# Optimization experiments

Measured on AMD Instinct MI355X. Metric: run time of the kernel, lower is better.

The kernel has to match this reference:

```python
import jax, jax.numpy as jnp
import numpy as np

B, T, C, HS = 4, 2048, 1024, 64

def setup_inputs() -> dict:
    key = jax.random.key(0)
    k1, k2, k3, k4 = jax.random.split(key, 4)
    # weights stored as [n_embd, head_size] so projection is x @ W
    scale = C ** -0.5
    return {
        "x": jax.random.normal(k1, (B, T, C), dtype=jnp.float32),
        "Wq": jax.random.normal(k2, (C, HS), dtype=jnp.float32) * scale,
        "Wk": jax.random.normal(k3, (C, HS), dtype=jnp.float32) * scale,
        "Wv": jax.random.normal(k4, (C, HS), dtype=jnp.float32) * scale,
    }

def reference(x, Wq, Wk, Wv):
    # single-head causal attention: softmax(QK^T / sqrt(hs)) V, dropout p=0 (eval)
    q = x @ Wq  # [B,T,hs]
    k = x @ Wk
    v = x @ Wv
    hs = k.shape[-1]
    wei = jnp.einsum('bqh,bkh->bqk', q, k) * (hs ** -0.5)  # [B,T,T]
    causal = jnp.tril(jnp.ones((q.shape[1], q.shape[1]), dtype=bool))
    wei = jnp.where(causal[None, :, :], wei, -jnp.inf)
    wei = jax.nn.softmax(wei, axis=-1)
    out = jnp.einsum('bqk,bkh->bqh', wei, v)  # [B,T,hs]
    return out
```

## Files before the change

### kernel.cpp

```cpp
#include <hip/hip_runtime.h>
#include <stdint.h>

#define NB 4
#define NT 2048
#define NC 1024
#define NH 64
#define NM (NB*NT)

typedef unsigned short u16;
typedef unsigned int u32;
typedef __bf16 bf16_t;
typedef float f32x4 __attribute__((ext_vector_type(4)));
typedef bf16_t bf16x8 __attribute__((ext_vector_type(8)));
typedef u16 u16x8 __attribute__((ext_vector_type(8)));
typedef u16 u16x4 __attribute__((ext_vector_type(4)));

__device__ __forceinline__ u16 f2b(float f) {
  return __builtin_bit_cast(u16, (bf16_t)f);
}

__device__ __forceinline__ void gl16(const void* g, void* l) {
  __builtin_amdgcn_global_load_lds(
      (const __attribute__((address_space(1))) u32*)g,
      (__attribute__((address_space(3))) u32*)l, 16, 0, 0);
}

__global__ __launch_bounds__(256) void wt_kernel(const float* __restrict__ Wq,
                                                 const float* __restrict__ Wk,
                                                 const float* __restrict__ Wv,
                                                 u16* __restrict__ wt) {
  __shared__ float t[64][65];
  const int m = blockIdx.x >> 4;
  const int kt = blockIdx.x & 15;
  const int k0 = kt * 64;
  const float* W = (m == 0) ? Wq : (m == 1) ? Wk : Wv;
  {
    const int r = threadIdx.x >> 2, c4 = threadIdx.x & 3;
    #pragma unroll
    for (int j = 0; j < 4; ++j) {
      const float4 f = *(const float4*)(W + (size_t)(k0 + r) * NH + c4 * 16 + j * 4);
      t[r][c4 * 16 + j * 4 + 0] = f.x;
      t[r][c4 * 16 + j * 4 + 1] = f.y;
      t[r][c4 * 16 + j * 4 + 2] = f.z;
      t[r][c4 * 16 + j * 4 + 3] = f.w;
    }
  }
  __syncthreads();
  const int n = threadIdx.x >> 2, kc = threadIdx.x & 3;
  u16x8 a, b;
  #pragma unroll
  for (int j = 0; j < 8; ++j) a[j] = f2b(t[kc * 16 + j][n]);
  #pragma unroll
  for (int j = 0; j < 8; ++j) b[j] = f2b(t[kc * 16 + 8 + j][n]);
  u16* dst = wt + ((size_t)(m * 64 + n)) * NC + k0 + kc * 16;
  *(u16x8*)dst = a;
  *(u16x8*)(dst + 8) = b;
}

__global__ __launch_bounds__(512) void proj_kernel(const float* __restrict__ x,
                                                   const u16* __restrict__ wt,
                                                   u16* __restrict__ qo,
                                                   u16* __restrict__ ko,
                                                   u16* __restrict__ vto) {
  __shared__ float fA[2][32 * 64];
  __shared__ u16 sB[2][64 * 64];
  const int tid = threadIdx.x;
  const int lane = tid & 63;
  const int wv = tid >> 6;
  const int rt = wv & 1;
  const int w = wv >> 1;
  const int g = lane >> 4;
  const int li = lane & 15;
  const int row0 = blockIdx.x * 32;
  const int m = blockIdx.y;
  const int wbase16 = (tid & 0x1C0) * 16;
  const u16* wslice = wt + (size_t)m * 64 * NC;

  const f32x4 zero = {0.f, 0.f, 0.f, 0.f};
  f32x4 acc = zero;

  const int ar = tid >> 4, ac = tid & 15;
  const int bn = tid >> 3, bc = tid & 7;
  const float* asrc = x + (size_t)(row0 + ar) * NC + ((ac ^ (ar & 7)) * 4);
  const u16* bsrc = wslice + (size_t)bn * NC + ((bc ^ (bn & 7)) * 8);

  auto stage = [&](int kt, int nxt) {
    const int k0 = kt * 64;
    gl16(asrc + k0, (char*)fA[nxt] + wbase16 + (lane << 4));
    gl16(bsrc + k0, (char*)sB[nxt] + wbase16 + (lane << 4));
  };

  stage(0, 0);
  __syncthreads();

  for (int kt = 0; kt < 16; ++kt) {
    const int cur = kt & 1;
    if (kt < 15) stage(kt + 1, cur ^ 1);
    #pragma unroll
    for (int ks = 0; ks < 2; ++ks) {
      const int n = w * 16 + li;
      const bf16x8 b = *(const bf16x8*)&sB[cur][n * 64 + (((ks * 4 + g) ^ (n & 7)) * 8)];
      const int r = rt * 16 + li;
      const int c0 = ks * 8 + g * 2;
      const f32x4 a0 = *(const f32x4*)&fA[cur][r * 64 + ((c0 ^ (r & 7)) * 4)];
      const f32x4 a1 = *(const f32x4*)&fA[cur][r * 64 + (((c0 + 1) ^ (r & 7)) * 4)];
      bf16x8 a;
      a[0]=(bf16_t)a0.x; a[1]=(bf16_t)a0.y; a[2]=(bf16_t)a0.z; a[3]=(bf16_t)a0.w;
      a[4]=(bf16_t)a1.x; a[5]=(bf16_t)a1.y; a[6]=(bf16_t)a1.z; a[7]=(bf16_t)a1.w;
      acc = __builtin_amdgcn_mfma_f32_16x16x32_bf16(a, b, acc, 0, 0, 0);
    }
    __syncthreads();
  }

  const int rr0 = row0 + rt * 16 + g * 4;
  if (m == 0) {
    #pragma unroll
    for (int i = 0; i < 4; ++i)
      qo[(size_t)(rr0 + i) * NH + w * 16 + li] = f2b(acc[i]);
  } else if (m == 1) {
    #pragma unroll
    for (int i = 0; i < 4; ++i)
      ko[(size_t)(rr0 + i) * NH + w * 16 + li] = f2b(acc[i]);
  } else {
    u16x4 pv;
    #pragma unroll
    for (int i = 0; i < 4; ++i) pv[i] = f2b(acc[i]);
    const int hs = w * 16 + li;
    const int bidx = rr0 >> 11;
    const int tt = rr0 & 2047;
    const int tile = tt >> 6, off = tt & 63;
    *(u16x4*)&vto[(((size_t)(bidx * 32 + tile) * 64) + hs) * 64 + off] = pv;
  }
}

struct AttnGrp {
  union {
    struct { u16 K[2][32 * 64]; u16 V[2][64 * 32]; } st;
    struct { float mo[2][16][64]; float ml[2][16]; } mg;
  } u;
};

__global__ __launch_bounds__(512) void attn_kernel(const u16* __restrict__ qg,
                                                   const u16* __restrict__ kg,
                                                   const u16* __restrict__ vtg,
                                                   float* __restrict__ out) {
  __shared__ AttnGrp grp[8];
  __shared__ u16 sP[8][16 * 32];
  const int tid = threadIdx.x;
  const int lane = tid & 63;
  const int s = tid >> 6;
  const int g = lane >> 4;
  const int li = lane & 15;
  const int jA = blockIdx.x & 63;
  const int bb = blockIdx.x >> 6;
  const int jB = 127 - jA;
  const size_t bt0 = (size_t)bb * NT;
  const int q0A = jA * 16, q0B = jB * 16;
  const int n1 = (jA >> 1) + 1;

  bf16x8 aqA[2], aqB[2];
  #pragma unroll
  for (int ks = 0; ks < 2; ++ks) {
    aqA[ks] = *(const bf16x8*)(qg + (bt0 + q0A + li) * NH + ks * 32 + g * 8);
    aqB[ks] = *(const bf16x8*)(qg + (bt0 + q0B + li) * NH + ks * 32 + g * 8);
  }

  const f32x4 zero = {0.f, 0.f, 0.f, 0.f};
  f32x4 oA[4], oB[4];
  float lA[4], lB[4];
  #pragma unroll
  for (int i = 0; i < 4; ++i) { oA[i] = zero; oB[i] = zero; lA[i] = 0.f; lB[i] = 0.f; }

  auto stageKV = [&](int v, int b) {
    const int kvt = (v < n1) ? v : v - n1;
    const size_t kbase = bt0 + (size_t)kvt * 32;
    #pragma unroll
    for (int jj = 0; jj < 4; ++jj) {
      const int idx = jj * 64 + lane;
      const int n = idx >> 3, c = idx & 7;
      gl16(kg + (kbase + n) * NH + ((c ^ (n & 7)) * 8),
           (char*)grp[s].u.st.K[b] + jj * 1024);
    }
    const size_t vbase = ((size_t)(bb * 32 + (kvt >> 1))) * 64;
    const int hoff = (kvt & 1) * 32;
    #pragma unroll
    for (int jj = 0; jj < 4; ++jj) {
      const int idx = jj * 64 + lane;
      const int n = idx >> 2, c = idx & 3;
      gl16(vtg + (vbase + n) * 64 + hoff + ((c ^ (n & 3) ^ ((n >> 2) & 3)) * 8),
           (char*)grp[s].u.st.V[b] + jj * 1024);
    }
  };

  auto computeT = [&](const bf16x8 (&aq)[2], f32x4 (&o)[4], float (&ls)[4],
                      int q0, int kv0, int b) {
    f32x4 sc2[2] = {zero, zero};
    #pragma unroll
    for (int ks = 0; ks < 2; ++ks) {
      #pragma unroll
      for (int fn = 0; fn < 2; ++fn) {
        const int n = fn * 16 + li;
        const bf16x8 bk = *(const bf16x8*)&grp[s].u.st.K[b][n * 64 + (((ks * 4 + g) ^ (n & 7)) * 8)];
        sc2[fn] = __builtin_amdgcn_mfma_f32_16x16x32_bf16(aq[ks], bk, sc2[fn], 0, 0, 0);
      }
    }
    const bool needmask = (kv0 + 31 > q0);
    #pragma unroll
    for (int fn = 0; fn < 2; ++fn) {
      #pragma unroll
      for (int i = 0; i < 4; ++i) {
        const int q = g * 4 + i;
        float v = sc2[fn][i] * 0.125f;
        if (needmask && (kv0 + fn * 16 + li > q0 + q)) v = -1e30f;
        const float e = __expf(v);
        ls[i] += e;
        const int kc = fn * 2 + (li >> 3);
        sP[s][q * 32 + ((kc ^ (q & 3) ^ ((q >> 2) & 3)) * 8) + (li & 7)] = f2b(e);
      }
    }
    const bf16x8 pa = *(const bf16x8*)&sP[s][li * 32 + ((g ^ (li & 3) ^ ((li >> 2) & 3)) * 8)];
    #pragma unroll
    for (int fn = 0; fn < 4; ++fn) {
      const int n = fn * 16 + li;
      const bf16x8 bv = *(const bf16x8*)&grp[s].u.st.V[b][n * 32 + ((g ^ (n & 3) ^ ((n >> 2) & 3)) * 8)];
      o[fn] = __builtin_amdgcn_mfma_f32_16x16x32_bf16(pa, bv, o[fn], 0, 0, 0);
    }
  };

  const int nt = (64 - s) / 8 + 1;
  int v = s;
  stageKV(v, 0);
  for (int k = 0; k < nt; ++k) {
    if (k + 1 < nt) {
      stageKV(v + 8, (k + 1) & 1);
      asm volatile("s_waitcnt vmcnt(8)" ::: "memory");
    } else {
      asm volatile("s_waitcnt vmcnt(0)" ::: "memory");
    }
    const int b = k & 1;
    if (v < n1) computeT(aqA, oA, lA, q0A, v * 32, b);
    else        computeT(aqB, oB, lB, q0B, (v - n1) * 32, b);
    v += 8;
  }

  #pragma unroll
  for (int i = 0; i < 4; ++i) {
    float a = lA[i], c = lB[i];
    a += __shfl_xor(a, 1); c += __shfl_xor(c, 1);
    a += __shfl_xor(a, 2); c += __shfl_xor(c, 2);
    a += __shfl_xor(a, 4); c += __shfl_xor(c, 4);
    a += __shfl_xor(a, 8); c += __shfl_xor(c, 8);
    lA[i] = a; lB[i] = c;
  }

  #pragma unroll
  for (int fn = 0; fn < 4; ++fn) {
    #pragma unroll
    for (int i = 0; i < 4; ++i) {
      grp[s].u.mg.mo[0][g * 4 + i][fn * 16 + li] = oA[fn][i];
      grp[s].u.mg.mo[1][g * 4 + i][fn * 16 + li] = oB[fn][i];
    }
  }
  if (li == 0) {
    #pragma unroll
    for (int i = 0; i < 4; ++i) {
      grp[s].u.mg.ml[0][g * 4 + i] = lA[i];
      grp[s].u.mg.ml[1][g * 4 + i] = lB[i];
    }
  }
  __syncthreads();

  {
    const int base = tid * 4;
    const int tile = base >> 10;
    const int r = (base >> 6) & 15;
    const int c0 = base & 63;
    float L = 0.f;
    f32x4 acc = zero;
    #pragma unroll
    for (int s8 = 0; s8 < 8; ++s8) {
      L += grp[s8].u.mg.ml[tile][r];
      acc += *(const f32x4*)&grp[s8].u.mg.mo[tile][r][c0];
    }
    const int row = (tile ? q0B : q0A) + r;
    const float inv = 1.f / L;
    acc *= inv;
    *(f32x4*)&out[(bt0 + row) * NH + c0] = acc;
  }
}

extern "C" void kernel_launch(void* const* d_in, const int* in_sizes, int n_in,
                              void* d_out, int out_size, void* d_ws, size_t ws_size,
                              hipStream_t stream) {
  (void)in_sizes; (void)n_in; (void)out_size; (void)ws_size;
  const float* x  = (const float*)d_in[0];
  const float* Wq = (const float*)d_in[1];
  const float* Wk = (const float*)d_in[2];
  const float* Wv = (const float*)d_in[3];
  float* out = (float*)d_out;
  char* ws = (char*)d_ws;
  u16* qb  = (u16*)(ws);
  u16* kb  = (u16*)(ws + (1u << 20));
  u16* vtb = (u16*)(ws + (2u << 20));
  u16* wtb = (u16*)(ws + (3u << 20));
  hipLaunchKernelGGL(wt_kernel,   dim3(48),     dim3(256), 0, stream, Wq, Wk, Wv, wtb);
  hipLaunchKernelGGL(proj_kernel, dim3(256, 3), dim3(512), 0, stream, x, wtb, qb, kb, vtb);
  hipLaunchKernelGGL(attn_kernel, dim3(256),    dim3(512), 0, stream, qb, kb, vtb, out);
}
```

Before: 35.41 us.

## Double attention waves per block and load V fragments directly to registers

The attention kernel goes from 8 to 16 waves per 1024-thread block, so each wave handles half as many KV tiles in its strided split. V is no longer staged through LDS; each wave loads its MFMA B-fragments for V straight from global memory into registers, while K keeps its double-buffered global-to-LDS path. The final merge now sums 16 partial results per row, with two scalar outputs per thread. This adds more waves to hide latency but raises register pressure at 1024 threads, issues uncoalesced direct V loads, and makes the cross-wave reduction longer.

```diff
diff --git a/kernel.cpp b/kernel.cpp
--- a/kernel.cpp
+++ b/kernel.cpp
@@ -135,17 +135,17 @@
 
 struct AttnGrp {
   union {
-    struct { u16 K[2][32 * 64]; u16 V[2][64 * 32]; } st;
+    u16 K[2][32 * 64];
     struct { float mo[2][16][64]; float ml[2][16]; } mg;
   } u;
 };
 
-__global__ __launch_bounds__(512) void attn_kernel(const u16* __restrict__ qg,
-                                                   const u16* __restrict__ kg,
-                                                   const u16* __restrict__ vtg,
-                                                   float* __restrict__ out) {
-  __shared__ AttnGrp grp[8];
-  __shared__ u16 sP[8][16 * 32];
+__global__ __launch_bounds__(1024) void attn_kernel(const u16* __restrict__ qg,
+                                                    const u16* __restrict__ kg,
+                                                    const u16* __restrict__ vtg,
+                                                    float* __restrict__ out) {
+  __shared__ AttnGrp grp[16];
+  __shared__ u16 sP[16][16 * 32];
   const int tid = threadIdx.x;
   const int lane = tid & 63;
   const int s = tid >> 6;
@@ -171,7 +171,7 @@
   #pragma unroll
   for (int i = 0; i < 4; ++i) { oA[i] = zero; oB[i] = zero; lA[i] = 0.f; lB[i] = 0.f; }
 
-  auto stageKV = [&](int v, int b) {
+  auto stageK = [&](int v, int b) {
     const int kvt = (v < n1) ? v : v - n1;
     const size_t kbase = bt0 + (size_t)kvt * 32;
     #pragma unroll
@@ -179,28 +179,19 @@
       const int idx = jj * 64 + lane;
       const int n = idx >> 3, c = idx & 7;
       gl16(kg + (kbase + n) * NH + ((c ^ (n & 7)) * 8),
-           (char*)grp[s].u.st.K[b] + jj * 1024);
-    }
-    const size_t vbase = ((size_t)(bb * 32 + (kvt >> 1))) * 64;
-    const int hoff = (kvt & 1) * 32;
-    #pragma unroll
-    for (int jj = 0; jj < 4; ++jj) {
-      const int idx = jj * 64 + lane;
-      const int n = idx >> 2, c = idx & 3;
-      gl16(vtg + (vbase + n) * 64 + hoff + ((c ^ (n & 3) ^ ((n >> 2) & 3)) * 8),
-           (char*)grp[s].u.st.V[b] + jj * 1024);
+           (char*)grp[s].u.K[b] + jj * 1024);
     }
   };
 
   auto computeT = [&](const bf16x8 (&aq)[2], f32x4 (&o)[4], float (&ls)[4],
-                      int q0, int kv0, int b) {
+                      int q0, int kv0, int b, const bf16x8 (&vf)[4]) {
     f32x4 sc2[2] = {zero, zero};
     #pragma unroll
     for (int ks = 0; ks < 2; ++ks) {
       #pragma unroll
       for (int fn = 0; fn < 2; ++fn) {
         const int n = fn * 16 + li;
-        const bf16x8 bk = *(const bf16x8*)&grp[s].u.st.K[b][n * 64 + (((ks * 4 + g) ^ (n & 7)) * 8)];
+        const bf16x8 bk = *(const bf16x8*)&grp[s].u.K[b][n * 64 + (((ks * 4 + g) ^ (n & 7)) * 8)];
         sc2[fn] = __builtin_amdgcn_mfma_f32_16x16x32_bf16(aq[ks], bk, sc2[fn], 0, 0, 0);
       }
     }
@@ -220,27 +211,30 @@
     }
     const bf16x8 pa = *(const bf16x8*)&sP[s][li * 32 + ((g ^ (li & 3) ^ ((li >> 2) & 3)) * 8)];
     #pragma unroll
-    for (int fn = 0; fn < 4; ++fn) {
-      const int n = fn * 16 + li;
-      const bf16x8 bv = *(const bf16x8*)&grp[s].u.st.V[b][n * 32 + ((g ^ (n & 3) ^ ((n >> 2) & 3)) * 8)];
-      o[fn] = __builtin_amdgcn_mfma_f32_16x16x32_bf16(pa, bv, o[fn], 0, 0, 0);
-    }
+    for (int fn = 0; fn < 4; ++fn)
+      o[fn] = __builtin_amdgcn_mfma_f32_16x16x32_bf16(pa, vf[fn], o[fn], 0, 0, 0);
   };
 
-  const int nt = (64 - s) / 8 + 1;
-  int v = s;
-  stageKV(v, 0);
-  for (int k = 0; k < nt; ++k) {
-    if (k + 1 < nt) {
-      stageKV(v + 8, (k + 1) & 1);
+  stageK(s, 0);
+  int k = 0;
+  for (int v = s; v < 65; v += 16, ++k) {
+    const int kvt = (v < n1) ? v : v - n1;
+    bf16x8 vf[4];
+    const size_t vrow = ((size_t)(bb * 32 + (kvt >> 1))) * 64;
+    const int hoff = (kvt & 1) * 32;
+    #pragma unroll
+    for (int fn = 0; fn < 4; ++fn)
+      vf[fn] = *(const bf16x8*)(vtg + (vrow + fn * 16 + li) * 64 + hoff + g * 8);
+
+    if (v + 16 < 65) {
+      stageK(v + 16, (k + 1) & 1);
       asm volatile("s_waitcnt vmcnt(8)" ::: "memory");
     } else {
-      asm volatile("s_waitcnt vmcnt(0)" ::: "memory");
+      asm volatile("s_waitcnt vmcnt(4)" ::: "memory");
     }
     const int b = k & 1;
-    if (v < n1) computeT(aqA, oA, lA, q0A, v * 32, b);
-    else        computeT(aqB, oB, lB, q0B, (v - n1) * 32, b);
-    v += 8;
+    if (v < n1) computeT(aqA, oA, lA, q0A, kvt * 32, b, vf);
+    else        computeT(aqB, oB, lB, q0B, kvt * 32, b, vf);
   }
 
   #pragma unroll
@@ -271,21 +265,22 @@
   __syncthreads();
 
   {
-    const int base = tid * 4;
+    const int base = tid * 2;
     const int tile = base >> 10;
     const int r = (base >> 6) & 15;
     const int c0 = base & 63;
     float L = 0.f;
-    f32x4 acc = zero;
-    #pragma unroll
-    for (int s8 = 0; s8 < 8; ++s8) {
-      L += grp[s8].u.mg.ml[tile][r];
-      acc += *(const f32x4*)&grp[s8].u.mg.mo[tile][r][c0];
+    float a0 = 0.f, a1 = 0.f;
+    #pragma unroll
+    for (int s16 = 0; s16 < 16; ++s16) {
+      L += grp[s16].u.mg.ml[tile][r];
+      a0 += grp[s16].u.mg.mo[tile][r][c0];
+      a1 += grp[s16].u.mg.mo[tile][r][c0 + 1];
     }
     const int row = (tile ? q0B : q0A) + r;
     const float inv = 1.f / L;
-    acc *= inv;
-    *(f32x4*)&out[(bt0 + row) * NH + c0] = acc;
+    out[(bt0 + row) * NH + c0] = a0 * inv;
+    out[(bt0 + row) * NH + c0 + 1] = a1 * inv;
   }
 }
 
@@ -303,7 +298,7 @@
   u16* kb  = (u16*)(ws + (1u << 20));
   u16* vtb = (u16*)(ws + (2u << 20));
   u16* wtb = (u16*)(ws + (3u << 20));
-  hipLaunchKernelGGL(wt_kernel,   dim3(48),     dim3(256), 0, stream, Wq, Wk, Wv, wtb);
-  hipLaunchKernelGGL(proj_kernel, dim3(256, 3), dim3(512), 0, stream, x, wtb, qb, kb, vtb);
-  hipLaunchKernelGGL(attn_kernel, dim3(256),    dim3(512), 0, stream, qb, kb, vtb, out);
-}
+  hipLaunchKernelGGL(wt_kernel,   dim3(48),     dim3(256),  0, stream, Wq, Wk, Wv, wtb);
+  hipLaunchKernelGGL(proj_kernel, dim3(256, 3), dim3(512),  0, stream, x, wtb, qb, kb, vtb);
+  hipLaunchKernelGGL(attn_kernel, dim3(256),    dim3(1024), 0, stream, qb, kb, vtb, out);
+}
```

After: 38.54 us. 8.8% more time.
